# Performance work log

Measured on AMD Instinct MI355X. Metric: run time of the kernel, lower is better.

The kernel has to match this reference:

```python
import jax, jax.numpy as jnp
import numpy as np

EPS = 1e-5

def setup_inputs() -> dict:
    key = jax.random.key(0)
    ks = jax.random.split(key, 9)
    N, D, L, C = 1, 128, 256, 256
    OC, PC = 32, 256
    msa_matrix = jax.random.normal(ks[0], (N, D, L, C), dtype=jnp.float32)
    ln_w = jnp.ones((C,), dtype=jnp.float32)
    ln_b = jnp.zeros((C,), dtype=jnp.float32)
    s = 1.0 / np.sqrt(C)
    Wl = jax.random.uniform(ks[1], (OC, C), dtype=jnp.float32, minval=-s, maxval=s)
    bl = jax.random.uniform(ks[2], (OC,), dtype=jnp.float32, minval=-s, maxval=s)
    Wr = jax.random.uniform(ks[3], (OC, C), dtype=jnp.float32, minval=-s, maxval=s)
    br = jax.random.uniform(ks[4], (OC,), dtype=jnp.float32, minval=-s, maxval=s)
    so = 1.0 / np.sqrt(OC * OC)
    Wout = jax.random.uniform(ks[5], (PC, OC * OC), dtype=jnp.float32, minval=-so, maxval=so)
    bout = jax.random.uniform(ks[6], (PC,), dtype=jnp.float32, minval=-so, maxval=so)
    return {"msa_matrix": msa_matrix, "ln_w": ln_w, "ln_b": ln_b,
            "Wl": Wl, "bl": bl, "Wr": Wr, "br": br, "Wout": Wout, "bout": bout}

def reference(msa_matrix, ln_w, ln_b, Wl, bl, Wr, br, Wout, bout):
    N, D, L, C = msa_matrix.shape
    OC = Wl.shape[0]
    # LayerNorm over channels
    mu = jnp.mean(msa_matrix, axis=-1, keepdims=True)
    var = jnp.var(msa_matrix, axis=-1, keepdims=True)
    x = (msa_matrix - mu) * jax.lax.rsqrt(var + EPS) * ln_w + ln_b
    # Dual projections: [N, D, L, OC]
    left = jnp.einsum('ndlc,oc->ndlo', x, Wl) + bl
    right = (jnp.einsum('ndlc,oc->ndlo', x, Wr) + br) / D
    # Outer-product mean over MSA depth: [N, L, L, OC, OC]
    outprod = jnp.einsum('ndlc,ndmq->nlmcq', left, right)
    outprod = outprod.reshape(N, L, L, OC * OC)
    # Output projection to pair channels
    return jnp.einsum('nlmk,pk->nlmp', outprod, Wout) + bout
```

## Files before the change

kernel.cpp:

```cpp
#include <hip/hip_runtime.h>

#define EPS 1e-5f

static constexpr int D  = 128;
static constexpr int L  = 256;
static constexpr int C  = 256;
static constexpr int OC = 32;
static constexpr int PC = 256;

typedef __attribute__((ext_vector_type(8))) short bfrag8;
typedef __attribute__((ext_vector_type(4))) short bhalf4;
typedef __attribute__((ext_vector_type(4))) float f32x4;
typedef __attribute__((ext_vector_type(4))) unsigned int u32x4;

__device__ inline unsigned short f2bf(float f) {
  union { float f; unsigned u; } v; v.f = f;
  unsigned r = v.u + 0x7FFF + ((v.u >> 16) & 1);
  return (unsigned short)(r >> 16);
}

__global__ __launch_bounds__(256, 4)
void prep_ln(const float* __restrict__ msa,
             const float* __restrict__ lnw, const float* __restrict__ lnb,
             const float* __restrict__ Wl, const float* __restrict__ Wr,
             const float* __restrict__ Wout,
             const float* __restrict__ bl, const float* __restrict__ br,
             unsigned short* __restrict__ Wbf3,
             unsigned short* __restrict__ leftT, unsigned short* __restrict__ rightT) {
  const int t = threadIdx.x;
  const int b = blockIdx.x;

  if (b < 64) {
    #pragma unroll
    for (int j2 = 0; j2 < 4; ++j2) {
      const int e0 = (b * 256 + t) * 16 + j2 * 4;
      const int lane = (e0 >> 3) & 63, ks = (e0 >> 9) & 31, pf = e0 >> 14;
      const int p = pf * 16 + (lane & 15);
      unsigned short v[4];
      #pragma unroll
      for (int j = 0; j < 4; ++j) {
        const int kp = ks * 32 + ((lane >> 4) * 8) + ((e0 + j) & 7);
        const int q = kp >> 5, t5 = kp & 31;
        const int cc = ((t5 >> 2) & 1) * 16 + (t5 >> 3) * 4 + (t5 & 3);
        v[j] = f2bf(Wout[p * 1024 + cc * 32 + q]);
      }
      *(bhalf4*)(Wbf3 + e0) = *(bhalf4*)v;
    }
    return;
  }

  __shared__ char xb[32768];

  const int bb = b - 64;
  const int lane = t & 63, w = t >> 6;
  const int d0 = (bb & 15) * 8, l0 = (bb >> 4) * 8;

  float4 xv[16];
  #pragma unroll
  for (int i = 0; i < 16; ++i) {
    const int r = i * 4 + w, dd = r & 7, ll = r >> 3;
    xv[i] = *(const float4*)(msa + ((size_t)(d0 + dd) * 256 + (l0 + ll)) * 256 + lane * 4);
  }

  bfrag8 wf[8];
  {
    const int n = w * 16 + (lane & 15);
    const int side = n >> 5, o = n & 31;
    const float* Wrow = (side ? Wr : Wl) + o * 256 + ((lane >> 4) * 8);
    #pragma unroll
    for (int ks = 0; ks < 8; ++ks) {
      const float4 w0 = *(const float4*)(Wrow + ks * 32);
      const float4 w1 = *(const float4*)(Wrow + ks * 32 + 4);
      unsigned short u[8];
      u[0] = f2bf(w0.x); u[1] = f2bf(w0.y); u[2] = f2bf(w0.z); u[3] = f2bf(w0.w);
      u[4] = f2bf(w1.x); u[5] = f2bf(w1.y); u[6] = f2bf(w1.z); u[7] = f2bf(w1.w);
      wf[ks] = *(bfrag8*)u;
    }
  }

  float mu[16], rs[16];
  #pragma unroll
  for (int i = 0; i < 16; ++i) {
    float s  = xv[i].x + xv[i].y + xv[i].z + xv[i].w;
    float s2 = xv[i].x * xv[i].x + xv[i].y * xv[i].y + xv[i].z * xv[i].z + xv[i].w * xv[i].w;
    #pragma unroll
    for (int off = 32; off >= 1; off >>= 1) {
      s  += __shfl_xor(s, off);
      s2 += __shfl_xor(s2, off);
    }
    mu[i] = s * (1.0f / C);
    rs[i] = rsqrtf(s2 * (1.0f / C) - mu[i] * mu[i] + EPS);
  }

  {
    const float4 wv = *(const float4*)(lnw + lane * 4);
    const float4 bv = *(const float4*)(lnb + lane * 4);
    #pragma unroll
    for (int i = 0; i < 16; ++i) {
      const int r = i * 4 + w;
      float4 v = xv[i];
      unsigned short u[4];
      u[0] = f2bf((v.x - mu[i]) * rs[i] * wv.x + bv.x);
      u[1] = f2bf((v.y - mu[i]) * rs[i] * wv.y + bv.y);
      u[2] = f2bf((v.z - mu[i]) * rs[i] * wv.z + bv.z);
      u[3] = f2bf((v.w - mu[i]) * rs[i] * wv.w + bv.w);
      *(bhalf4*)&xb[r * 512 + ((lane * 8) ^ ((r & 7) << 4))] = *(bhalf4*)u;
    }
  }
  __syncthreads();

  f32x4 acc[4];
  #pragma unroll
  for (int mf = 0; mf < 4; ++mf) acc[mf] = (f32x4)0.f;
  #pragma unroll
  for (int ks = 0; ks < 8; ++ks) {
    #pragma unroll
    for (int mf = 0; mf < 4; ++mf) {
      const int row = mf * 16 + (lane & 15);
      const bfrag8 af = *(const bfrag8*)&xb[row * 512 +
                          ((ks * 64 + ((lane >> 4) << 4)) ^ ((row & 7) << 4))];
      acc[mf] = __builtin_amdgcn_mfma_f32_16x16x32_bf16(af, wf[ks], acc[mf], 0, 0, 0);
    }
  }

  {
    const int n = w * 16 + (lane & 15);
    const int side = n >> 5, o = n & 31;
    const float bias = side ? br[o] : bl[o];
    const float sc = side ? (1.0f / D) : 1.0f;
    unsigned short* dst = side ? rightT : leftT;
    #pragma unroll
    for (int mf = 0; mf < 4; ++mf) {
      const int rbase = mf * 16 + ((lane >> 4) << 2);
      const int ll = rbase >> 3, ddb = rbase & 7;
      unsigned short u[4];
      #pragma unroll
      for (int r = 0; r < 4; ++r) u[r] = f2bf((acc[mf][r] + bias) * sc);
      *(bhalf4*)(dst + ((size_t)(l0 + ll) * 32 + o) * 128 + d0 + ddb) = *(bhalf4*)u;
    }
  }
}

__global__ __launch_bounds__(512, 4)
void fused_mfma(const unsigned short* __restrict__ leftT,
                const unsigned short* __restrict__ rightT,
                const unsigned short* __restrict__ Wbf3,
                const float* __restrict__ bout,
                float* __restrict__ out) {
  __shared__ char smem[65536];

  const int flat = blockIdx.x;
  const int wg = (flat & 7) * 256 + (flat >> 3);
  const int mt = wg & 31, lt = wg >> 5;
  const int l0 = lt * 4, m0 = mt * 8;

  const char* Aslab = (const char*)(leftT  + (size_t)l0 * 32 * 128);
  const char* Bslab = (const char*)(rightT + (size_t)m0 * 32 * 128);

  const int tid = threadIdx.x, lane = tid & 63, w = tid >> 6;
  const int wr = w >> 2, wc = w & 3;

  f32x4 acc[4][4];
  #pragma unroll
  for (int i = 0; i < 4; ++i)
    #pragma unroll
    for (int j = 0; j < 4; ++j) acc[i][j] = (f32x4)0.f;

  auto stageA = [&](int kh, int dst) {
    #pragma unroll
    for (int i = 0; i < 2; ++i) {
      const int lb = (i * 512 + tid) * 16;
      const int row = lb >> 7;
      const int sb = (lb & 127) ^ ((row & 7) << 4);
      __builtin_amdgcn_global_load_lds((const void*)(Aslab + (size_t)row * 256 + kh * 128 + sb),
                                       (void*)&smem[dst + lb], 16, 0, 0);
    }
  };
  auto stageB = [&](int kh) {
    #pragma unroll
    for (int i = 0; i < 4; ++i) {
      const int lb = (i * 512 + tid) * 16;
      const int row = lb >> 7;
      const int sb = (lb & 127) ^ ((row & 7) << 4);
      __builtin_amdgcn_global_load_lds((const void*)(Bslab + (size_t)row * 256 + kh * 128 + sb),
                                       (void*)&smem[16384 + lb], 16, 0, 0);
    }
  };
  auto computeKh = [&](int abase) {
    #pragma unroll
    for (int ks = 0; ks < 2; ++ks) {
      const int kb = ks * 64 + ((lane >> 4) << 4);
      bfrag8 a[4], b[4];
      #pragma unroll
      for (int i = 0; i < 4; ++i) {
        const int row = wr * 64 + i * 16 + (lane & 15);
        a[i] = *(const bfrag8*)&smem[abase + (row << 7) + (kb ^ ((row & 7) << 4))];
      }
      #pragma unroll
      for (int j = 0; j < 4; ++j) {
        const int row = wc * 64 + j * 16 + (lane & 15);
        b[j] = *(const bfrag8*)&smem[16384 + (row << 7) + (kb ^ ((row & 7) << 4))];
      }
      #pragma unroll
      for (int i = 0; i < 4; ++i)
        #pragma unroll
        for (int j = 0; j < 4; ++j)
          acc[i][j] = __builtin_amdgcn_mfma_f32_16x16x32_bf16(a[i], b[j], acc[i][j], 0, 0, 0);
    }
  };

  stageA(0, 0);
  stageB(0);
  __syncthreads();
  stageA(1, 49152);
  u32x4 b1r[4];
  #pragma unroll
  for (int i = 0; i < 4; ++i) {
    const int lb = (i * 512 + tid) * 16;
    const int row = lb >> 7;
    const int sb = (lb & 127) ^ ((row & 7) << 4);
    b1r[i] = *(const u32x4*)(Bslab + (size_t)row * 256 + 128 + sb);
  }
  computeKh(0);
  __syncthreads();
  #pragma unroll
  for (int i = 0; i < 4; ++i)
    *(u32x4*)&smem[16384 + (i * 512 + tid) * 16] = b1r[i];
  __syncthreads();
  computeKh(49152);
  __syncthreads();

  {
    const int c2_16 = (lane >> 4) << 4;
    #pragma unroll
    for (int ip = 0; ip < 2; ++ip) {
      const int ll = wr * 2 + ip;
      #pragma unroll
      for (int j = 0; j < 4; ++j) {
        const int col = wc * 64 + j * 16 + (lane & 15);
        const int mm = col >> 5, q = col & 31;
        const int pair = ll * 8 + mm;
        const int S = (pair & 7) ^ ((q >> 1) & 7);
        const int byte = pair * 2048 + ((q * 64 + c2_16) ^ (S << 4));
        u32x4 u;
        u[0] = (unsigned)f2bf(acc[2 * ip][j][0])     | ((unsigned)f2bf(acc[2 * ip][j][1]) << 16);
        u[1] = (unsigned)f2bf(acc[2 * ip][j][2])     | ((unsigned)f2bf(acc[2 * ip][j][3]) << 16);
        u[2] = (unsigned)f2bf(acc[2 * ip + 1][j][0]) | ((unsigned)f2bf(acc[2 * ip + 1][j][1]) << 16);
        u[3] = (unsigned)f2bf(acc[2 * ip + 1][j][2]) | ((unsigned)f2bf(acc[2 * ip + 1][j][3]) << 16);
        *(u32x4*)&smem[byte] = u;
      }
    }
  }

  const unsigned short* wp0 = Wbf3 + (((size_t)(w * 2)     * 32) * 64 + lane) * 8;
  const unsigned short* wp1 = Wbf3 + (((size_t)(w * 2 + 1) * 32) * 64 + lane) * 8;

  bfrag8 wfs[4][2];
  #pragma unroll
  for (int s = 0; s < 4; ++s) {
    wfs[s][0] = *(const bfrag8*)(wp0 + s * 512);
    wfs[s][1] = *(const bfrag8*)(wp1 + s * 512);
  }
  __syncthreads();

  f32x4 oacc[2][2];
  #pragma unroll
  for (int u = 0; u < 2; ++u)
    #pragma unroll
    for (int pj = 0; pj < 2; ++pj) oacc[u][pj] = (f32x4)0.f;

  auto ldos = [&](int ks, bfrag8* o) {
    #pragma unroll
    for (int pj = 0; pj < 2; ++pj) {
      const int pair = pj * 16 + (lane & 15);
      const int S = (pair & 7) ^ ((ks >> 1) & 7);
      o[pj] = *(const bfrag8*)&smem[pair * 2048 + ((ks * 64 + ((lane >> 4) << 4)) ^ (S << 4))];
    }
  };

  bfrag8 osf[4][2];
  ldos(0, osf[0]);
  ldos(1, osf[1]);
  ldos(2, osf[2]);

  #pragma unroll
  for (int ks = 0; ks < 32; ++ks) {
    if (ks + 3 < 32) ldos(ks + 3, osf[(ks + 3) & 3]);
    __builtin_amdgcn_s_setprio(1);
    oacc[0][0] = __builtin_amdgcn_mfma_f32_16x16x32_bf16(wfs[ks & 3][0], osf[ks & 3][0], oacc[0][0], 0, 0, 0);
    oacc[0][1] = __builtin_amdgcn_mfma_f32_16x16x32_bf16(wfs[ks & 3][0], osf[ks & 3][1], oacc[0][1], 0, 0, 0);
    oacc[1][0] = __builtin_amdgcn_mfma_f32_16x16x32_bf16(wfs[ks & 3][1], osf[ks & 3][0], oacc[1][0], 0, 0, 0);
    oacc[1][1] = __builtin_amdgcn_mfma_f32_16x16x32_bf16(wfs[ks & 3][1], osf[ks & 3][1], oacc[1][1], 0, 0, 0);
    __builtin_amdgcn_s_setprio(0);
    if (ks + 4 < 32) {
      wfs[ks & 3][0] = *(const bfrag8*)(wp0 + (ks + 4) * 512);
      wfs[ks & 3][1] = *(const bfrag8*)(wp1 + (ks + 4) * 512);
    }
  }

  {
    #pragma unroll
    for (int u = 0; u < 2; ++u) {
      const int p0 = (w * 2 + u) * 16 + ((lane >> 4) << 2);
      const float4 bb = *(const float4*)&bout[p0];
      #pragma unroll
      for (int pj = 0; pj < 2; ++pj) {
        const int pair = pj * 16 + (lane & 15);
        const int ll = pair >> 3, mm = pair & 7;
        float4 v;
        v.x = oacc[u][pj][0] + bb.x;
        v.y = oacc[u][pj][1] + bb.y;
        v.z = oacc[u][pj][2] + bb.z;
        v.w = oacc[u][pj][3] + bb.w;
        *(float4*)&out[((size_t)(l0 + ll) * L + (m0 + mm)) * PC + p0] = v;
      }
    }
  }
}

extern "C" void kernel_launch(void* const* d_in, const int* in_sizes, int n_in,
                              void* d_out, int out_size, void* d_ws, size_t ws_size,
                              hipStream_t stream) {
  const float* msa  = (const float*)d_in[0];
  const float* ln_w = (const float*)d_in[1];
  const float* ln_b = (const float*)d_in[2];
  const float* Wl   = (const float*)d_in[3];
  const float* bl   = (const float*)d_in[4];
  const float* Wr   = (const float*)d_in[5];
  const float* br   = (const float*)d_in[6];
  const float* Wout = (const float*)d_in[7];
  const float* bout = (const float*)d_in[8];
  float* out = (float*)d_out;

  unsigned short* leftT  = (unsigned short*)d_ws;
  unsigned short* rightT = leftT + (size_t)L * 32 * 128;
  unsigned short* Wbf3   = rightT + (size_t)L * 32 * 128;

  prep_ln<<<dim3(576), 256, 0, stream>>>(msa, ln_w, ln_b, Wl, Wr, Wout, bl, br,
                                         Wbf3, leftT, rightT);
  fused_mfma<<<dim3(2048), 512, 0, stream>>>(leftT, rightT, Wbf3, bout, out);
}
```

Measured before the change: 81.82 us.

## Make fused MFMA kernel persistent, looping over m-tiles with resident A slab

Launches 256 blocks instead of 2048; each block keeps both K-halves of its left slab in LDS and iterates over 8 consecutive m-tiles. The next tile's first B half is prefetched into LDS during the output projection of the current tile. This removes redundant A loads and per-block launch overhead but doubles LDS to 128KB, limiting residency to one block per CU and reducing latency hiding.

Measured after the change: 241.6 us. 2.95x slower.

```diff
diff --git a/kernel.cpp b/kernel.cpp
--- a/kernel.cpp
+++ b/kernel.cpp
@@ -141,30 +141,26 @@
   }
 }
 
-__global__ __launch_bounds__(512, 4)
+__global__ __launch_bounds__(512, 2)
 void fused_mfma(const unsigned short* __restrict__ leftT,
                 const unsigned short* __restrict__ rightT,
                 const unsigned short* __restrict__ Wbf3,
                 const float* __restrict__ bout,
                 float* __restrict__ out) {
-  __shared__ char smem[65536];
-
-  const int flat = blockIdx.x;
-  const int wg = (flat & 7) * 256 + (flat >> 3);
-  const int mt = wg & 31, lt = wg >> 5;
-  const int l0 = lt * 4, m0 = mt * 8;
-
-  const char* Aslab = (const char*)(leftT  + (size_t)l0 * 32 * 128);
-  const char* Bslab = (const char*)(rightT + (size_t)m0 * 32 * 128);
+  __shared__ char smem[131072];
+
+  const int b = blockIdx.x;
+  const int swz = (b & 7) * 32 + (b >> 3);
+  const int lt = swz >> 2;
+  const int mtBase = (swz & 3) * 8;
+  const int l0 = lt * 4;
+
+  const char* Aslab = (const char*)(leftT + (size_t)l0 * 32 * 128);
 
   const int tid = threadIdx.x, lane = tid & 63, w = tid >> 6;
   const int wr = w >> 2, wc = w & 3;
 
-  f32x4 acc[4][4];
-  #pragma unroll
-  for (int i = 0; i < 4; ++i)
-    #pragma unroll
-    for (int j = 0; j < 4; ++j) acc[i][j] = (f32x4)0.f;
+  constexpr int OS0 = 0, BB = 65536, A0 = 98304, A1 = 114688;
 
   auto stageA = [&](int kh, int dst) {
     #pragma unroll
@@ -176,145 +172,165 @@
                                        (void*)&smem[dst + lb], 16, 0, 0);
     }
   };
-  auto stageB = [&](int kh) {
+  auto stageB0 = [&](const char* Bslab) {
     #pragma unroll
     for (int i = 0; i < 4; ++i) {
       const int lb = (i * 512 + tid) * 16;
       const int row = lb >> 7;
       const int sb = (lb & 127) ^ ((row & 7) << 4);
-      __builtin_amdgcn_global_load_lds((const void*)(Bslab + (size_t)row * 256 + kh * 128 + sb),
-                                       (void*)&smem[16384 + lb], 16, 0, 0);
+      __builtin_amdgcn_global_load_lds((const void*)(Bslab + (size_t)row * 256 + sb),
+                                       (void*)&smem[BB + lb], 16, 0, 0);
     }
   };
-  auto computeKh = [&](int abase) {
-    #pragma unroll
-    for (int ks = 0; ks < 2; ++ks) {
-      const int kb = ks * 64 + ((lane >> 4) << 4);
-      bfrag8 a[4], b[4];
-      #pragma unroll
-      for (int i = 0; i < 4; ++i) {
-        const int row = wr * 64 + i * 16 + (lane & 15);
-        a[i] = *(const bfrag8*)&smem[abase + (row << 7) + (kb ^ ((row & 7) << 4))];
-      }
-      #pragma unroll
-      for (int j = 0; j < 4; ++j) {
-        const int row = wc * 64 + j * 16 + (lane & 15);
-        b[j] = *(const bfrag8*)&smem[16384 + (row << 7) + (kb ^ ((row & 7) << 4))];
-      }
-      #pragma unroll
-      for (int i = 0; i < 4; ++i)
-        #pragma unroll
-        for (int j = 0; j < 4; ++j)
-          acc[i][j] = __builtin_amdgcn_mfma_f32_16x16x32_bf16(a[i], b[j], acc[i][j], 0, 0, 0);
-    }
-  };
-
-  stageA(0, 0);
-  stageB(0);
+
+  const char* Bslab = (const char*)(rightT + (size_t)(mtBase) * 8 * 32 * 128);
+  stageA(0, A0);
+  stageA(1, A1);
+  stageB0(Bslab);
   __syncthreads();
-  stageA(1, 49152);
-  u32x4 b1r[4];
-  #pragma unroll
-  for (int i = 0; i < 4; ++i) {
-    const int lb = (i * 512 + tid) * 16;
-    const int row = lb >> 7;
-    const int sb = (lb & 127) ^ ((row & 7) << 4);
-    b1r[i] = *(const u32x4*)(Bslab + (size_t)row * 256 + 128 + sb);
-  }
-  computeKh(0);
-  __syncthreads();
-  #pragma unroll
-  for (int i = 0; i < 4; ++i)
-    *(u32x4*)&smem[16384 + (i * 512 + tid) * 16] = b1r[i];
-  __syncthreads();
-  computeKh(49152);
-  __syncthreads();
-
-  {
-    const int c2_16 = (lane >> 4) << 4;
-    #pragma unroll
-    for (int ip = 0; ip < 2; ++ip) {
-      const int ll = wr * 2 + ip;
-      #pragma unroll
-      for (int j = 0; j < 4; ++j) {
-        const int col = wc * 64 + j * 16 + (lane & 15);
-        const int mm = col >> 5, q = col & 31;
-        const int pair = ll * 8 + mm;
-        const int S = (pair & 7) ^ ((q >> 1) & 7);
-        const int byte = pair * 2048 + ((q * 64 + c2_16) ^ (S << 4));
-        u32x4 u;
-        u[0] = (unsigned)f2bf(acc[2 * ip][j][0])     | ((unsigned)f2bf(acc[2 * ip][j][1]) << 16);
-        u[1] = (unsigned)f2bf(acc[2 * ip][j][2])     | ((unsigned)f2bf(acc[2 * ip][j][3]) << 16);
-        u[2] = (unsigned)f2bf(acc[2 * ip + 1][j][0]) | ((unsigned)f2bf(acc[2 * ip + 1][j][1]) << 16);
-        u[3] = (unsigned)f2bf(acc[2 * ip + 1][j][2]) | ((unsigned)f2bf(acc[2 * ip + 1][j][3]) << 16);
-        *(u32x4*)&smem[byte] = u;
-      }
-    }
-  }
-
-  const unsigned short* wp0 = Wbf3 + (((size_t)(w * 2)     * 32) * 64 + lane) * 8;
-  const unsigned short* wp1 = Wbf3 + (((size_t)(w * 2 + 1) * 32) * 64 + lane) * 8;
-
-  bfrag8 wfs[4][2];
-  #pragma unroll
-  for (int s = 0; s < 4; ++s) {
-    wfs[s][0] = *(const bfrag8*)(wp0 + s * 512);
-    wfs[s][1] = *(const bfrag8*)(wp1 + s * 512);
-  }
-  __syncthreads();
-
-  f32x4 oacc[2][2];
-  #pragma unroll
-  for (int u = 0; u < 2; ++u)
-    #pragma unroll
-    for (int pj = 0; pj < 2; ++pj) oacc[u][pj] = (f32x4)0.f;
-
-  auto ldos = [&](int ks, bfrag8* o) {
-    #pragma unroll
-    for (int pj = 0; pj < 2; ++pj) {
-      const int pair = pj * 16 + (lane & 15);
-      const int S = (pair & 7) ^ ((ks >> 1) & 7);
-      o[pj] = *(const bfrag8*)&smem[pair * 2048 + ((ks * 64 + ((lane >> 4) << 4)) ^ (S << 4))];
-    }
-  };
-
-  bfrag8 osf[4][2];
-  ldos(0, osf[0]);
-  ldos(1, osf[1]);
-  ldos(2, osf[2]);
-
-  #pragma unroll
-  for (int ks = 0; ks < 32; ++ks) {
-    if (ks + 3 < 32) ldos(ks + 3, osf[(ks + 3) & 3]);
-    __builtin_amdgcn_s_setprio(1);
-    oacc[0][0] = __builtin_amdgcn_mfma_f32_16x16x32_bf16(wfs[ks & 3][0], osf[ks & 3][0], oacc[0][0], 0, 0, 0);
-    oacc[0][1] = __builtin_amdgcn_mfma_f32_16x16x32_bf16(wfs[ks & 3][0], osf[ks & 3][1], oacc[0][1], 0, 0, 0);
-    oacc[1][0] = __builtin_amdgcn_mfma_f32_16x16x32_bf16(wfs[ks & 3][1], osf[ks & 3][0], oacc[1][0], 0, 0, 0);
-    oacc[1][1] = __builtin_amdgcn_mfma_f32_16x16x32_bf16(wfs[ks & 3][1], osf[ks & 3][1], oacc[1][1], 0, 0, 0);
-    __builtin_amdgcn_s_setprio(0);
-    if (ks + 4 < 32) {
-      wfs[ks & 3][0] = *(const bfrag8*)(wp0 + (ks + 4) * 512);
-      wfs[ks & 3][1] = *(const bfrag8*)(wp1 + (ks + 4) * 512);
-    }
-  }
-
-  {
-    #pragma unroll
-    for (int u = 0; u < 2; ++u) {
-      const int p0 = (w * 2 + u) * 16 + ((lane >> 4) << 2);
-      const float4 bb = *(const float4*)&bout[p0];
+
+  for (int t = 0; t < 8; ++t) {
+    const int mt = mtBase + t;
+    const int m0 = mt * 8;
+
+    f32x4 acc[4][4];
+    #pragma unroll
+    for (int i = 0; i < 4; ++i)
+      #pragma unroll
+      for (int j = 0; j < 4; ++j) acc[i][j] = (f32x4)0.f;
+
+    auto computeKh = [&](int abase) {
+      #pragma unroll
+      for (int ks = 0; ks < 2; ++ks) {
+        const int kb = ks * 64 + ((lane >> 4) << 4);
+        bfrag8 a[4], bfr[4];
+        #pragma unroll
+        for (int i = 0; i < 4; ++i) {
+          const int row = wr * 64 + i * 16 + (lane & 15);
+          a[i] = *(const bfrag8*)&smem[abase + (row << 7) + (kb ^ ((row & 7) << 4))];
+        }
+        #pragma unroll
+        for (int j = 0; j < 4; ++j) {
+          const int row = wc * 64 + j * 16 + (lane & 15);
+          bfr[j] = *(const bfrag8*)&smem[BB + (row << 7) + (kb ^ ((row & 7) << 4))];
+        }
+        #pragma unroll
+        for (int i = 0; i < 4; ++i)
+          #pragma unroll
+          for (int j = 0; j < 4; ++j)
+            acc[i][j] = __builtin_amdgcn_mfma_f32_16x16x32_bf16(a[i], bfr[j], acc[i][j], 0, 0, 0);
+      }
+    };
+
+    u32x4 b1r[4];
+    #pragma unroll
+    for (int i = 0; i < 4; ++i) {
+      const int lb = (i * 512 + tid) * 16;
+      const int row = lb >> 7;
+      const int sb = (lb & 127) ^ ((row & 7) << 4);
+      b1r[i] = *(const u32x4*)(Bslab + (size_t)row * 256 + 128 + sb);
+    }
+    computeKh(A0);
+    __syncthreads();
+    #pragma unroll
+    for (int i = 0; i < 4; ++i)
+      *(u32x4*)&smem[BB + (i * 512 + tid) * 16] = b1r[i];
+    __syncthreads();
+    computeKh(A1);
+
+    {
+      const int c2_16 = (lane >> 4) << 4;
+      #pragma unroll
+      for (int ip = 0; ip < 2; ++ip) {
+        const int ll = wr * 2 + ip;
+        #pragma unroll
+        for (int j = 0; j < 4; ++j) {
+          const int col = wc * 64 + j * 16 + (lane & 15);
+          const int mm = col >> 5, q = col & 31;
+          const int pair = ll * 8 + mm;
+          const int S = (pair & 7) ^ ((q >> 1) & 7);
+          const int byte = pair * 2048 + ((q * 64 + c2_16) ^ (S << 4));
+          u32x4 u;
+          u[0] = (unsigned)f2bf(acc[2 * ip][j][0])     | ((unsigned)f2bf(acc[2 * ip][j][1]) << 16);
+          u[1] = (unsigned)f2bf(acc[2 * ip][j][2])     | ((unsigned)f2bf(acc[2 * ip][j][3]) << 16);
+          u[2] = (unsigned)f2bf(acc[2 * ip + 1][j][0]) | ((unsigned)f2bf(acc[2 * ip + 1][j][1]) << 16);
+          u[3] = (unsigned)f2bf(acc[2 * ip + 1][j][2]) | ((unsigned)f2bf(acc[2 * ip + 1][j][3]) << 16);
+          *(u32x4*)&smem[OS0 + byte] = u;
+        }
+      }
+    }
+    __syncthreads();
+
+    if (t + 1 < 8) {
+      Bslab = (const char*)(rightT + (size_t)(mt + 1) * 8 * 32 * 128);
+      stageB0(Bslab);
+    }
+
+    const unsigned short* wp0 = Wbf3 + (((size_t)(w * 2)     * 32) * 64 + lane) * 8;
+    const unsigned short* wp1 = Wbf3 + (((size_t)(w * 2 + 1) * 32) * 64 + lane) * 8;
+
+    bfrag8 wfs[4][2];
+    #pragma unroll
+    for (int s = 0; s < 4; ++s) {
+      wfs[s][0] = *(const bfrag8*)(wp0 + s * 512);
+      wfs[s][1] = *(const bfrag8*)(wp1 + s * 512);
+    }
+
+    f32x4 oacc[2][2];
+    #pragma unroll
+    for (int u = 0; u < 2; ++u)
+      #pragma unroll
+      for (int pj = 0; pj < 2; ++pj) oacc[u][pj] = (f32x4)0.f;
+
+    auto ldos = [&](int ks, bfrag8* o) {
       #pragma unroll
       for (int pj = 0; pj < 2; ++pj) {
         const int pair = pj * 16 + (lane & 15);
-        const int ll = pair >> 3, mm = pair & 7;
-        float4 v;
-        v.x = oacc[u][pj][0] + bb.x;
-        v.y = oacc[u][pj][1] + bb.y;
-        v.z = oacc[u][pj][2] + bb.z;
-        v.w = oacc[u][pj][3] + bb.w;
-        *(float4*)&out[((size_t)(l0 + ll) * L + (m0 + mm)) * PC + p0] = v;
-      }
-    }
+        const int S = (pair & 7) ^ ((ks >> 1) & 7);
+        o[pj] = *(const bfrag8*)&smem[OS0 + pair * 2048 +
+                   ((ks * 64 + ((lane >> 4) << 4)) ^ (S << 4))];
+      }
+    };
+
+    bfrag8 osf[4][2];
+    ldos(0, osf[0]);
+    ldos(1, osf[1]);
+    ldos(2, osf[2]);
+
+    #pragma unroll
+    for (int ks = 0; ks < 32; ++ks) {
+      if (ks + 3 < 32) ldos(ks + 3, osf[(ks + 3) & 3]);
+      __builtin_amdgcn_s_setprio(1);
+      oacc[0][0] = __builtin_amdgcn_mfma_f32_16x16x32_bf16(wfs[ks & 3][0], osf[ks & 3][0], oacc[0][0], 0, 0, 0);
+      oacc[0][1] = __builtin_amdgcn_mfma_f32_16x16x32_bf16(wfs[ks & 3][0], osf[ks & 3][1], oacc[0][1], 0, 0, 0);
+      oacc[1][0] = __builtin_amdgcn_mfma_f32_16x16x32_bf16(wfs[ks & 3][1], osf[ks & 3][0], oacc[1][0], 0, 0, 0);
+      oacc[1][1] = __builtin_amdgcn_mfma_f32_16x16x32_bf16(wfs[ks & 3][1], osf[ks & 3][1], oacc[1][1], 0, 0, 0);
+      __builtin_amdgcn_s_setprio(0);
+      if (ks + 4 < 32) {
+        wfs[ks & 3][0] = *(const bfrag8*)(wp0 + (ks + 4) * 512);
+        wfs[ks & 3][1] = *(const bfrag8*)(wp1 + (ks + 4) * 512);
+      }
+    }
+
+    {
+      #pragma unroll
+      for (int u = 0; u < 2; ++u) {
+        const int p0 = (w * 2 + u) * 16 + ((lane >> 4) << 2);
+        const float4 bb = *(const float4*)&bout[p0];
+        #pragma unroll
+        for (int pj = 0; pj < 2; ++pj) {
+          const int pair = pj * 16 + (lane & 15);
+          const int ll = pair >> 3, mm = pair & 7;
+          float4 v;
+          v.x = oacc[u][pj][0] + bb.x;
+          v.y = oacc[u][pj][1] + bb.y;
+          v.z = oacc[u][pj][2] + bb.z;
+          v.w = oacc[u][pj][3] + bb.w;
+          *(float4*)&out[((size_t)(l0 + ll) * L + (m0 + mm)) * PC + p0] = v;
+        }
+      }
+    }
+    __syncthreads();
   }
 }
 
@@ -338,5 +354,5 @@
 
   prep_ln<<<dim3(576), 256, 0, stream>>>(msa, ln_w, ln_b, Wl, Wr, Wout, bl, br,
                                          Wbf3, leftT, rightT);
-  fused_mfma<<<dim3(2048), 512, 0, stream>>>(leftT, rightT, Wbf3, bout, out);
+  fused_mfma<<<dim3(256), 512, 0, stream>>>(leftT, rightT, Wbf3, bout, out);
 }
```
